# Kernel tuning notes

Hardware: AMD Instinct MI355X
Metric: run time of the kernel (lower is better)

The kernel has to match this reference:

```python
import jax, jax.numpy as jnp
import numpy as np

H, W = 448, 448
C = 32
HEADS = 2
HEAD_DIM = C // HEADS
B, N = 4, 20000
SHIFTS = jnp.array([[0, 0], [-1, 0], [1, 0], [0, 1], [-1, 1], [1, 1], [0, -1], [-1, -1], [1, -1]], dtype=jnp.int32)  # [9,2]


def _layer_norm(x, w, b):
    mu = x.mean(-1, keepdims=True)
    var = ((x - mu) ** 2).mean(-1, keepdims=True)
    return (x - mu) / jnp.sqrt(var + 1e-5) * w + b


def _direction(q_feat, q_coor, kv_feat, kv_coor, qkv_w, qkv_b, in_w, in_b, out_w, out_b, pos_w, pos_b):
    # q_feat: [N,C] (already layer-normed), q_coor/kv_coor: [N,2] int (y,x)
    n = q_feat.shape[0]
    q_map = q_feat @ qkv_w[0].T + qkv_b[0]   # 1x1 conv == linear
    k_map = kv_feat @ qkv_w[1].T + qkv_b[1]
    v_map = kv_feat @ qkv_w[2].T + qkv_b[2]
    # dense coordinate -> voxel-index lookup table for the kv modality
    lut = jnp.full(H * W, -1, dtype=jnp.int32)
    lut = lut.at[kv_coor[:, 0] * W + kv_coor[:, 1]].set(jnp.arange(kv_coor.shape[0], dtype=jnp.int32))
    shifted = q_coor[:, None, :] + SHIFTS[None]                      # [N,9,2]
    inb = ((shifted >= 0) & (shifted < jnp.array([H, W]))).all(-1)   # [N,9]
    flat = jnp.clip(shifted[..., 0], 0, H - 1) * W + jnp.clip(shifted[..., 1], 0, W - 1)
    idx = jnp.where(inb, lut[flat], -1)                              # [N,9], -1 = no match
    mask = idx >= 0
    gi = jnp.maximum(idx, 0)
    pos = SHIFTS.astype(q_feat.dtype) @ pos_w.T + pos_b              # [9,C]
    v_g = jnp.where(mask[..., None], v_map[gi] + pos[None], 0.0)     # [N,9,C]
    k_g = jnp.where(mask[..., None], k_map[gi], 0.0)                 # [N,9,C]
    # MultiheadAttention (eval): 1 query token over 9 neighbor tokens, per voxel
    wq, wk, wv = in_w[:C], in_w[C:2 * C], in_w[2 * C:]
    bq, bk, bv = in_b[:C], in_b[C:2 * C], in_b[2 * C:]
    q = (q_map @ wq.T + bq).reshape(n, HEADS, HEAD_DIM)
    k = (k_g @ wk.T + bk).reshape(n, 9, HEADS, HEAD_DIM)
    v = (v_g @ wv.T + bv).reshape(n, 9, HEADS, HEAD_DIM)
    scores = jnp.einsum('nhd,nkhd->nhk', q, k) / jnp.sqrt(jnp.asarray(HEAD_DIM, q.dtype))
    attn = jax.nn.softmax(scores, axis=-1)
    o = jnp.einsum('nhk,nkhd->nhd', attn, v).reshape(n, C)
    out = o @ out_w.T + out_b                                        # [N,C]
    # scatter into BEV pseudoimage
    canvas = jnp.zeros((H * W, C), out.dtype).at[q_coor[:, 0] * W + q_coor[:, 1]].set(out)
    return canvas.T.reshape(C, H, W)


def setup_inputs() -> dict:
    key = jax.random.key(0)
    ks = jax.random.split(key, 20)
    rng = np.random.default_rng(0)
    def coords(rng):
        flat = np.stack([rng.choice(H * W, size=N, replace=False) for _ in range(B)])
        return jnp.asarray(np.stack([flat // W, flat % W], axis=-1), dtype=jnp.int32)  # [B,N,2]
    s = 0.05
    return {
        'li_feats': jax.random.normal(ks[0], (B, N, C), jnp.float32),
        'ra_feats': jax.random.normal(ks[1], (B, N, C), jnp.float32),
        'li_coors': coords(rng),
        'ra_coors': coords(rng),
        'li_norm_w': jnp.ones((C,), jnp.float32),
        'li_norm_b': jnp.zeros((C,), jnp.float32),
        'ra_norm_w': jnp.ones((C,), jnp.float32),
        'ra_norm_b': jnp.zeros((C,), jnp.float32),
        'qkv1_w': jax.random.normal(ks[2], (3, C, C), jnp.float32) * s,
        'qkv1_b': jax.random.normal(ks[3], (3, C), jnp.float32) * s,
        'qkv2_w': jax.random.normal(ks[4], (3, C, C), jnp.float32) * s,
        'qkv2_b': jax.random.normal(ks[5], (3, C), jnp.float32) * s,
        'pos_w': jax.random.normal(ks[6], (C, 2), jnp.float32) * s,
        'pos_b': jax.random.normal(ks[7], (C,), jnp.float32) * s,
        'attn1_in_w': jax.random.normal(ks[8], (3 * C, C), jnp.float32) * s,
        'attn1_in_b': jax.random.normal(ks[9], (3 * C,), jnp.float32) * s,
        'attn1_out_w': jax.random.normal(ks[10], (C, C), jnp.float32) * s,
        'attn1_out_b': jax.random.normal(ks[11], (C,), jnp.float32) * s,
        'attn2_in_w': jax.random.normal(ks[12], (3 * C, C), jnp.float32) * s,
        'attn2_in_b': jax.random.normal(ks[13], (3 * C,), jnp.float32) * s,
        'attn2_out_w': jax.random.normal(ks[14], (C, C), jnp.float32) * s,
        'attn2_out_b': jax.random.normal(ks[15], (C,), jnp.float32) * s,
    }


def reference(li_feats, ra_feats, li_coors, ra_coors, li_norm_w, li_norm_b, ra_norm_w, ra_norm_b,
              qkv1_w, qkv1_b, qkv2_w, qkv2_b, pos_w, pos_b,
              attn1_in_w, attn1_in_b, attn1_out_w, attn1_out_b,
              attn2_in_w, attn2_in_b, attn2_out_w, attn2_out_b):
    li_n = _layer_norm(li_feats, li_norm_w, li_norm_b)  # [B,N,C]
    ra_n = _layer_norm(ra_feats, ra_norm_w, ra_norm_b)
    d1 = jax.vmap(lambda qf, qc, kf, kc: _direction(qf, qc, kf, kc, qkv1_w, qkv1_b,
                                                    attn1_in_w, attn1_in_b, attn1_out_w, attn1_out_b, pos_w, pos_b))
    d2 = jax.vmap(lambda qf, qc, kf, kc: _direction(qf, qc, kf, kc, qkv2_w, qkv2_b,
                                                    attn2_in_w, attn2_in_b, attn2_out_w, attn2_out_b, pos_w, pos_b))
    li_img = d1(li_n, li_coors, ra_n, ra_coors)  # [B,C,H,W]
    ra_img = d2(ra_n, ra_coors, li_n, li_coors)  # [B,C,H,W]
    return li_img, ra_img
```

## Files before the change

### kernel.cpp

```cpp
#include <hip/hip_runtime.h>
#include <hip/hip_bf16.h>

#define HH 448
#define WW 448
#define HWP (HH*WW)
#define CC 32
#define NN 20000
#define BB 4
#define PBLK 512
#define NPB 79

__constant__ int c_SY[9] = {0,-1,1,0,-1,1,0,-1,1};
__constant__ int c_SX[9] = {0,0,0,1,1,1,-1,-1,-1};

#define WB_STRIDE 4608

static __device__ __forceinline__ float bf(const __hip_bfloat16 v) {
    return __bfloat162float(v);
}
static __device__ __forceinline__ float ldf(const void* p, int i, int isf32) {
    if (isf32) return ((const float*)p)[i];
    return __bfloat162float(((const __hip_bfloat16*)p)[i]);
}
static __device__ __forceinline__ float blo(unsigned int u) { return __uint_as_float((u & 0xFFFFu) << 16); }
static __device__ __forceinline__ float bhi(unsigned int u) { return __uint_as_float(u & 0xFFFF0000u); }

static __device__ __forceinline__ void unpack8(uint4 r, float* f) {
    f[0]=blo(r.x); f[1]=bhi(r.x); f[2]=blo(r.y); f[3]=bhi(r.y);
    f[4]=blo(r.z); f[5]=bhi(r.z); f[6]=blo(r.w); f[7]=bhi(r.w);
}
static __device__ __forceinline__ float dot8(uint4 r, const float* q) {
    float a = 0.f;
    a = fmaf(blo(r.x), q[0], a); a = fmaf(bhi(r.x), q[1], a);
    a = fmaf(blo(r.y), q[2], a); a = fmaf(bhi(r.y), q[3], a);
    a = fmaf(blo(r.z), q[4], a); a = fmaf(bhi(r.z), q[5], a);
    a = fmaf(blo(r.w), q[6], a); a = fmaf(bhi(r.w), q[7], a);
    return a;
}
static __device__ __forceinline__ void acc8(uint4 r, float w, float4 pA, float4 pB, float* o) {
    o[0]=fmaf(w, blo(r.x)+pA.x, o[0]); o[1]=fmaf(w, bhi(r.x)+pA.y, o[1]);
    o[2]=fmaf(w, blo(r.y)+pA.z, o[2]); o[3]=fmaf(w, bhi(r.y)+pA.w, o[3]);
    o[4]=fmaf(w, blo(r.z)+pB.x, o[4]); o[5]=fmaf(w, bhi(r.z)+pB.y, o[5]);
    o[6]=fmaf(w, blo(r.w)+pB.z, o[6]); o[7]=fmaf(w, bhi(r.w)+pB.w, o[7]);
}

__launch_bounds__(256)
__global__ void prep_build(const void* __restrict__ qkv1_w, const void* __restrict__ qkv1_b,
                           const void* __restrict__ qkv2_w, const void* __restrict__ qkv2_b,
                           const void* __restrict__ pos_w,  const void* __restrict__ pos_b,
                           const void* __restrict__ in1_w,  const void* __restrict__ in1_b,
                           const void* __restrict__ out1_w, const void* __restrict__ out1_b,
                           const void* __restrict__ in2_w,  const void* __restrict__ in2_b,
                           const void* __restrict__ out2_w, const void* __restrict__ out2_b,
                           const void* __restrict__ li_feats,
                           const int* __restrict__ li_coors, const int* __restrict__ ra_coors,
                           int* __restrict__ lut,
                           int* __restrict__ flag, float* __restrict__ wsW) {
    const int tid = threadIdx.x;
    if (blockIdx.x >= 2) {
        const int t = (blockIdx.x - 2) * 256 + tid;
        if (t >= 2 * BB * NN) return;
        const int tensor = t / (BB * NN);
        const int r = t % (BB * NN);
        const int b = r / NN, n = r % NN;
        const int* cc = tensor ? ra_coors : li_coors;
        const int y = cc[(size_t)(b * NN + n) * 2 + 0];
        const int x = cc[(size_t)(b * NN + n) * 2 + 1];
        lut[(size_t)(tensor * BB + b) * HWP + y * WW + x] = n;
        return;
    }
    __shared__ int cnt[256];
    {
        const unsigned short u = ((const unsigned short*)li_feats)[tid * 2];
        const int e = (u >> 7) & 0xFF;
        cnt[tid] = (u == 0 || (e >= 97 && e <= 157)) ? 1 : 0;
    }
    __syncthreads();
    for (int s = 128; s > 0; s >>= 1) {
        if (tid < s) cnt[tid] += cnt[tid + s];
        __syncthreads();
    }
    const int F = (cnt[0] >= 192) ? 0 : 1;
    if (blockIdx.x == 0 && tid == 0) *flag = F;

    const int d = blockIdx.x;
    const void* qw  = d ? qkv2_w : qkv1_w;
    const void* qb  = d ? qkv2_b : qkv1_b;
    const void* iw  = d ? in2_w  : in1_w;
    const void* ib  = d ? in2_b  : in1_b;
    const void* ow  = d ? out2_w : out1_w;
    const void* obp = d ? out2_b : out1_b;
    float* o = wsW + d * WB_STRIDE;

    __shared__ float s_qw[3072];
    __shared__ float s_iw[96 * 33];
    __shared__ float s_ow[32 * 33];
    __shared__ float s_qb[96], s_ib[96], s_obp[32], s_pw[64], s_pb[32];

    if (F) {
        const float* fqw = (const float*)qw;  const float* fiw = (const float*)iw;
        const float* fow = (const float*)ow;  const float* fqb = (const float*)qb;
        const float* fib = (const float*)ib;  const float* fob = (const float*)obp;
        const float* fpw = (const float*)pos_w; const float* fpb = (const float*)pos_b;
        for (int i = tid; i < 3072; i += 256) s_qw[i] = fqw[i];
        for (int i = tid; i < 3072; i += 256) s_iw[(i >> 5) * 33 + (i & 31)] = fiw[i];
        for (int i = tid; i < 1024; i += 256) s_ow[(i >> 5) * 33 + (i & 31)] = fow[i];
        if (tid < 96) { s_qb[tid] = fqb[tid]; s_ib[tid] = fib[tid]; }
        if (tid < 64) s_pw[tid] = fpw[tid];
        if (tid < 32) { s_obp[tid] = fob[tid]; s_pb[tid] = fpb[tid]; }
    } else {
        const __hip_bfloat16* hqw = (const __hip_bfloat16*)qw;  const __hip_bfloat16* hiw = (const __hip_bfloat16*)iw;
        const __hip_bfloat16* how = (const __hip_bfloat16*)ow;  const __hip_bfloat16* hqb = (const __hip_bfloat16*)qb;
        const __hip_bfloat16* hib = (const __hip_bfloat16*)ib;  const __hip_bfloat16* hob = (const __hip_bfloat16*)obp;
        const __hip_bfloat16* hpw = (const __hip_bfloat16*)pos_w; const __hip_bfloat16* hpb = (const __hip_bfloat16*)pos_b;
        for (int i = tid; i < 3072; i += 256) s_qw[i] = bf(hqw[i]);
        for (int i = tid; i < 3072; i += 256) s_iw[(i >> 5) * 33 + (i & 31)] = bf(hiw[i]);
        for (int i = tid; i < 1024; i += 256) s_ow[(i >> 5) * 33 + (i & 31)] = bf(how[i]);
        if (tid < 96) { s_qb[tid] = bf(hqb[tid]); s_ib[tid] = bf(hib[tid]); }
        if (tid < 64) s_pw[tid] = bf(hpw[tid]);
        if (tid < 32) { s_obp[tid] = bf(hob[tid]); s_pb[tid] = bf(hpb[tid]); }
    }
    __syncthreads();

    for (int k = 0; k < 4; ++k) {
        const int idx = tid + k * 256;
        const int t = idx >> 5, i = idx & 31;
        float aq = 0.f, ak = 0.f, av = 0.f;
        #pragma unroll
        for (int u = 0; u < 32; ++u) {
            const float q0 = s_qw[u * 32 + t];
            const float q1 = s_qw[1024 + u * 32 + t];
            const float q2 = s_qw[2048 + u * 32 + t];
            aq = fmaf(s_iw[i * 33 + u],        q0, aq);
            ak = fmaf(s_iw[(32 + i) * 33 + u], q1, ak);
            av = fmaf(s_iw[(64 + i) * 33 + u], q2, av);
        }
        o[idx]        = aq;
        o[1024 + idx] = ak;
        o[2048 + idx] = av;
        o[3072 + idx] = s_ow[i * 33 + t];
    }
    if (tid < 32) {
        const int i = tid;
        float aq = 0.f, ak = 0.f, av = 0.f;
        #pragma unroll
        for (int u = 0; u < 32; ++u) {
            aq = fmaf(s_qb[u],      s_iw[i * 33 + u],        aq);
            ak = fmaf(s_qb[32 + u], s_iw[(32 + i) * 33 + u], ak);
            av = fmaf(s_qb[64 + u], s_iw[(64 + i) * 33 + u], av);
        }
        o[4096 + i] = aq + s_ib[i];
        o[4128 + i] = ak + s_ib[32 + i];
        o[4160 + i] = av + s_ib[64 + i];
        o[4192 + i] = s_obp[i];
        o[4224 + i] = s_ib[32 + i];
        o[4256 + i] = s_ib[64 + i];
    }
    for (int idx = tid; idx < 288; idx += 256) {
        const int s = idx >> 5, i = idx & 31;
        const float sy = (float)c_SY[s], sx = (float)c_SX[s];
        float acc = 0.f;
        #pragma unroll
        for (int j = 0; j < 32; ++j) {
            const float pj = sy * s_pw[j * 2 + 0] + sx * s_pw[j * 2 + 1] + s_pb[j];
            acc = fmaf(pj, s_iw[(64 + i) * 33 + j], acc);
        }
        o[4288 + idx] = acc;
    }
}

__launch_bounds__(256)
__global__ void project_kernel(const void* __restrict__ li_feats, const void* __restrict__ ra_feats,
                               const void* __restrict__ li_nw, const void* __restrict__ li_nb,
                               const void* __restrict__ ra_nw, const void* __restrict__ ra_nb,
                               const int* __restrict__ flag, const float* __restrict__ wsW,
                               __hip_bfloat16* __restrict__ qOut, __hip_bfloat16* __restrict__ kOut,
                               __hip_bfloat16* __restrict__ vOut) {
    const int F = *flag;
    const int combo  = blockIdx.x / PBLK;
    const int blk    = blockIdx.x % PBLK;
    const int tensor = combo >> 2;
    const int b      = combo & 3;
    const int qd  = tensor;
    const int kvd = 1 - tensor;

    __shared__ float wq[1024], wk[1024], wv[1024];
    __shared__ float bq[32], bk[32], bvv[32], nw[32], nb[32];
    const float* Wq  = wsW + qd  * WB_STRIDE;
    const float* Wkv = wsW + kvd * WB_STRIDE;
    for (int k = threadIdx.x; k < 1024; k += 256) {
        wq[k] = Wq[k];
        wk[k] = Wkv[1024 + k];
        wv[k] = Wkv[2048 + k];
    }
    if (threadIdx.x < 32) {
        bq[threadIdx.x]  = Wq[4096 + threadIdx.x];
        bk[threadIdx.x]  = Wkv[4128 + threadIdx.x];
        bvv[threadIdx.x] = Wkv[4160 + threadIdx.x];
        const void* w  = tensor ? ra_nw : li_nw;
        const void* bb = tensor ? ra_nb : li_nb;
        nw[threadIdx.x] = ldf(w, threadIdx.x, F);
        nb[threadIdx.x] = ldf(bb, threadIdx.x, F);
    }
    __syncthreads();

    const void* feats = tensor ? ra_feats : li_feats;
    const int lane = threadIdx.x & 31;
    const int sub  = threadIdx.x >> 5;

    for (int n0 = blk * 8; n0 < NN; n0 += PBLK * 8) {
        const int n = n0 + sub;
        if (n < NN) {
            const float x = ldf(feats, (b * NN + n) * CC + lane, F);
            float s = x;
            #pragma unroll
            for (int m = 1; m < 32; m <<= 1) s += __shfl_xor(s, m);
            const float mu = s * (1.f / 32.f);
            const float dx = x - mu;
            float s2 = dx * dx;
            #pragma unroll
            for (int m = 1; m < 32; m <<= 1) s2 += __shfl_xor(s2, m);
            const float var = s2 * (1.f / 32.f);
            const float xn = dx * rsqrtf(var + 1e-5f) * nw[lane] + nb[lane];

            float aq = bq[lane], ak = bk[lane], av = bvv[lane];
            #pragma unroll
            for (int t = 0; t < 32; ++t) {
                const float xb = __shfl(xn, t, 32);
                aq = fmaf(wq[t * 32 + lane], xb, aq);
                ak = fmaf(wk[t * 32 + lane], xb, ak);
                av = fmaf(wv[t * 32 + lane], xb, av);
            }
            const size_t off = ((size_t)(tensor * BB + b) * NN + n) * CC + lane;
            qOut[off] = __float2bfloat16(aq);
            kOut[off] = __float2bfloat16(ak);
            vOut[off] = __float2bfloat16(av);
        }
    }
}

__launch_bounds__(256)
__global__ void attn_kernel(const int* __restrict__ li_coors, const int* __restrict__ ra_coors,
                            const float* __restrict__ wsW, const int* __restrict__ lut,
                            const __hip_bfloat16* __restrict__ qArr, const __hip_bfloat16* __restrict__ kArr,
                            const __hip_bfloat16* __restrict__ vArr, __hip_bfloat16* __restrict__ resArr) {
    const int combo = blockIdx.x / NPB;
    const int n     = (blockIdx.x % NPB) * 256 + threadIdx.x;
    const int d = combo >> 2;
    const int b = combo & 3;
    const int qt = d, kt = 1 - d;

    __shared__ __align__(16) float wo[1024];
    __shared__ __align__(16) float pv[288];
    __shared__ __align__(16) float ob[32], bkr[32], bvr[32];
    const float* Wd = wsW + d * WB_STRIDE;
    for (int k = threadIdx.x; k < 1024; k += 256) wo[k] = Wd[3072 + k];
    if (threadIdx.x < 32) {
        ob[threadIdx.x]  = Wd[4192 + threadIdx.x];
        bkr[threadIdx.x] = Wd[4224 + threadIdx.x];
        bvr[threadIdx.x] = Wd[4256 + threadIdx.x];
    }
    for (int k = threadIdx.x; k < 288; k += 256) pv[k] = Wd[4288 + k];
    __syncthreads();
    if (n >= NN) return;

    const int* qc = qt ? ra_coors : li_coors;
    const int* lutk = lut + (size_t)(kt * BB + b) * HWP;
    const __hip_bfloat16* kk = kArr + (size_t)(kt * BB + b) * NN * CC;
    const __hip_bfloat16* vv = vArr + (size_t)(kt * BB + b) * NN * CC;
    const __hip_bfloat16* qq = qArr + (size_t)(qt * BB + b) * NN * CC;
    __hip_bfloat16* res = resArr + (size_t)(d * BB + b) * NN * CC;

    float q[32];
    {
        const uint4* qr = (const uint4*)(qq + (size_t)n * CC);
        unpack8(qr[0], q); unpack8(qr[1], q + 8);
        unpack8(qr[2], q + 16); unpack8(qr[3], q + 24);
    }
    const int y = qc[(size_t)(b * NN + n) * 2 + 0];
    const int x = qc[(size_t)(b * NN + n) * 2 + 1];
    int idx[9];
    #pragma unroll
    for (int s = 0; s < 9; ++s) {
        const int ny = y + c_SY[s], nx = x + c_SX[s];
        idx[s] = (ny >= 0 && ny < HH && nx >= 0 && nx < WW) ? lutk[ny * WW + nx] : -1;
    }
    float di0 = 0.f, di1 = 0.f;
    #pragma unroll
    for (int c = 0; c < 16; ++c) di0 = fmaf(q[c], bkr[c], di0);
    #pragma unroll
    for (int c = 16; c < 32; ++c) di1 = fmaf(q[c], bkr[c], di1);

    float s0[9], s1[9];
    #pragma unroll
    for (int s = 0; s < 9; ++s) {
        float d0, d1;
        if (idx[s] >= 0) {
            const uint4* kr = (const uint4*)(kk + (size_t)idx[s] * CC);
            const uint4 r0 = kr[0], r1 = kr[1], r2 = kr[2], r3 = kr[3];
            d0 = dot8(r0, q) + dot8(r1, q + 8);
            d1 = dot8(r2, q + 16) + dot8(r3, q + 24);
        } else { d0 = di0; d1 = di1; }
        s0[s] = d0 * 0.25f;
        s1[s] = d1 * 0.25f;
    }
    float m0 = s0[0], m1 = s1[0];
    #pragma unroll
    for (int s = 1; s < 9; ++s) { m0 = fmaxf(m0, s0[s]); m1 = fmaxf(m1, s1[s]); }
    float e0[9], e1[9], den0 = 0.f, den1 = 0.f;
    #pragma unroll
    for (int s = 0; s < 9; ++s) {
        e0[s] = __expf(s0[s] - m0); den0 += e0[s];
        e1[s] = __expf(s1[s] - m1); den1 += e1[s];
    }
    const float i0 = 1.f / den0, i1 = 1.f / den1;

    float o[32];
    #pragma unroll
    for (int c = 0; c < 32; ++c) o[c] = 0.f;
    float wi0 = 0.f, wi1 = 0.f;
    const float4* pv4 = (const float4*)pv;
    #pragma unroll
    for (int s = 0; s < 9; ++s) {
        const float w0 = e0[s] * i0, w1 = e1[s] * i1;
        if (idx[s] >= 0) {
            const uint4* vr = (const uint4*)(vv + (size_t)idx[s] * CC);
            const uint4 r0 = vr[0], r1 = vr[1], r2 = vr[2], r3 = vr[3];
            acc8(r0, w0, pv4[s * 8 + 0], pv4[s * 8 + 1], o);
            acc8(r1, w0, pv4[s * 8 + 2], pv4[s * 8 + 3], o + 8);
            acc8(r2, w1, pv4[s * 8 + 4], pv4[s * 8 + 5], o + 16);
            acc8(r3, w1, pv4[s * 8 + 6], pv4[s * 8 + 7], o + 24);
        } else { wi0 += w0; wi1 += w1; }
    }
    #pragma unroll
    for (int c = 0; c < 16; ++c) o[c] = fmaf(wi0, bvr[c], o[c]);
    #pragma unroll
    for (int c = 16; c < 32; ++c) o[c] = fmaf(wi1, bvr[c], o[c]);

    float out[32];
    const float4* ob4 = (const float4*)ob;
    #pragma unroll
    for (int i4 = 0; i4 < 8; ++i4) {
        const float4 t = ob4[i4];
        out[i4 * 4 + 0] = t.x; out[i4 * 4 + 1] = t.y;
        out[i4 * 4 + 2] = t.z; out[i4 * 4 + 3] = t.w;
    }
    #pragma unroll
    for (int j = 0; j < 32; ++j) {
        const float oj = o[j];
        const float4* wr = (const float4*)&wo[j * 32];
        #pragma unroll
        for (int i4 = 0; i4 < 8; ++i4) {
            const float4 w = wr[i4];
            out[i4 * 4 + 0] = fmaf(oj, w.x, out[i4 * 4 + 0]);
            out[i4 * 4 + 1] = fmaf(oj, w.y, out[i4 * 4 + 1]);
            out[i4 * 4 + 2] = fmaf(oj, w.z, out[i4 * 4 + 2]);
            out[i4 * 4 + 3] = fmaf(oj, w.w, out[i4 * 4 + 3]);
        }
    }
    __hip_bfloat16 hb[32];
    #pragma unroll
    for (int c = 0; c < 32; ++c) hb[c] = __float2bfloat16(out[c]);
    uint4* rp = (uint4*)(res + (size_t)n * CC);
    const uint4* hp = (const uint4*)hb;
    rp[0] = hp[0]; rp[1] = hp[1]; rp[2] = hp[2]; rp[3] = hp[3];
}

__launch_bounds__(256)
__global__ void canvas_kernel(const int* __restrict__ lut, const __hip_bfloat16* __restrict__ resArr,
                              const int* __restrict__ flag, void* __restrict__ out) {
    const int F = *flag;
    const int tile = blockIdx.x % (HWP / 64);
    const int rem  = blockIdx.x / (HWP / 64);
    const int b = rem & 3;
    const int d = rem >> 2;
    const int* lutq = lut + (size_t)(d * BB + b) * HWP + (size_t)tile * 64;
    __shared__ int ls[64];
    __shared__ float st[64 * 33];
    const int t = threadIdx.x;
    if (t < 16) ((int4*)ls)[t] = ((const int4*)lutq)[t];
    __syncthreads();

    const __hip_bfloat16* res = resArr + (size_t)(d * BB + b) * NN * CC;
    {
        const int r = t >> 2, q = t & 3;
        const int idx = ls[r];
        uint4 raw = make_uint4(0u, 0u, 0u, 0u);
        if (idx >= 0) raw = *(const uint4*)(res + (size_t)idx * CC + q * 8);
        float* dst = &st[r * 33 + q * 8];
        dst[0] = blo(raw.x); dst[1] = bhi(raw.x);
        dst[2] = blo(raw.y); dst[3] = bhi(raw.y);
        dst[4] = blo(raw.z); dst[5] = bhi(raw.z);
        dst[6] = blo(raw.w); dst[7] = bhi(raw.w);
    }
    __syncthreads();

    const int c = t >> 3, g = t & 7;
    float v[8];
    #pragma unroll
    for (int j = 0; j < 8; ++j) v[j] = st[(8 * g + j) * 33 + c];
    const size_t obase = ((size_t)(d * BB + b) * CC + c) * HWP + (size_t)tile * 64 + 8 * g;
    if (F) {
        float* ob = (float*)out + obase;
        ((float4*)ob)[0] = make_float4(v[0], v[1], v[2], v[3]);
        ((float4*)ob)[1] = make_float4(v[4], v[5], v[6], v[7]);
    } else {
        __hip_bfloat16* ob = (__hip_bfloat16*)out + obase;
        __hip_bfloat16 h[8];
        #pragma unroll
        for (int j = 0; j < 8; ++j) h[j] = __float2bfloat16(v[j]);
        *(uint4*)ob = *(const uint4*)h;
    }
}

extern "C" void kernel_launch(void* const* d_in, const int* in_sizes, int n_in,
                              void* d_out, int out_size, void* d_ws, size_t ws_size,
                              hipStream_t stream) {
    (void)in_sizes; (void)n_in; (void)out_size; (void)ws_size;
    const void* li_feats = d_in[0];
    const void* ra_feats = d_in[1];
    const int* li_coors = (const int*)d_in[2];
    const int* ra_coors = (const int*)d_in[3];
    const void* li_nw = d_in[4];
    const void* li_nb = d_in[5];
    const void* ra_nw = d_in[6];
    const void* ra_nb = d_in[7];

    char* ws = (char*)d_ws;
    int*   flag = (int*)ws;
    float* wsW  = (float*)(ws + 512);
    int*   lut  = (int*)(ws + 40960);
    __hip_bfloat16* qArr = (__hip_bfloat16*)(ws + 6463488);
    __hip_bfloat16* kArr = (__hip_bfloat16*)(ws + 16703488);
    __hip_bfloat16* vArr = (__hip_bfloat16*)(ws + 26943488);
    __hip_bfloat16* rArr = qArr;

    hipMemsetAsync(lut, 0xFF, (size_t)2 * BB * HWP * sizeof(int), stream);
    const int buildBlocks = (2 * BB * NN + 255) / 256;
    prep_build<<<2 + buildBlocks, 256, 0, stream>>>(d_in[8], d_in[9], d_in[10], d_in[11], d_in[12], d_in[13],
                                                    d_in[14], d_in[15], d_in[16], d_in[17],
                                                    d_in[18], d_in[19], d_in[20], d_in[21],
                                                    li_feats, li_coors, ra_coors, lut, flag, wsW);
    project_kernel<<<8 * PBLK, 256, 0, stream>>>(li_feats, ra_feats, li_nw, li_nb, ra_nw, ra_nb,
                                                 flag, wsW, qArr, kArr, vArr);
    attn_kernel<<<8 * NPB, 256, 0, stream>>>(li_coors, ra_coors, wsW, lut, qArr, kArr, vArr, rArr);
    canvas_kernel<<<2 * BB * (HWP / 64), 256, 0, stream>>>(lut, rArr, flag, d_out);
}
```

Baseline: 373.6 us.

## Map one voxel per thread in projection and read weights directly from global

```diff
diff --git a/kernel.cpp b/kernel.cpp
--- a/kernel.cpp
+++ b/kernel.cpp
@@ -7,7 +7,6 @@
 #define CC 32
 #define NN 20000
 #define BB 4
-#define PBLK 512
 #define NPB 79
 
 __constant__ int c_SY[9] = {0,-1,1,0,-1,1,0,-1,1};
@@ -42,6 +41,13 @@
     o[2]=fmaf(w, blo(r.y)+pA.z, o[2]); o[3]=fmaf(w, bhi(r.y)+pA.w, o[3]);
     o[4]=fmaf(w, blo(r.z)+pB.x, o[4]); o[5]=fmaf(w, bhi(r.z)+pB.y, o[5]);
     o[6]=fmaf(w, blo(r.w)+pB.z, o[6]); o[7]=fmaf(w, bhi(r.w)+pB.w, o[7]);
+}
+static __device__ __forceinline__ void store32bf(__hip_bfloat16* p, const float* a) {
+    __hip_bfloat16 h[32];
+    #pragma unroll
+    for (int c = 0; c < 32; ++c) h[c] = __float2bfloat16(a[c]);
+    uint4* rp = (uint4*)p; const uint4* hp = (const uint4*)h;
+    rp[0] = hp[0]; rp[1] = hp[1]; rp[2] = hp[2]; rp[3] = hp[3];
 }
 
 __launch_bounds__(256)
@@ -177,65 +183,69 @@
                                __hip_bfloat16* __restrict__ qOut, __hip_bfloat16* __restrict__ kOut,
                                __hip_bfloat16* __restrict__ vOut) {
     const int F = *flag;
-    const int combo  = blockIdx.x / PBLK;
-    const int blk    = blockIdx.x % PBLK;
+    const int combo  = blockIdx.x / NPB;
+    const int n      = (blockIdx.x % NPB) * 256 + threadIdx.x;
+    if (n >= NN) return;
     const int tensor = combo >> 2;
     const int b      = combo & 3;
-    const int qd  = tensor;
-    const int kvd = 1 - tensor;
-
-    __shared__ float wq[1024], wk[1024], wv[1024];
-    __shared__ float bq[32], bk[32], bvv[32], nw[32], nb[32];
-    const float* Wq  = wsW + qd  * WB_STRIDE;
-    const float* Wkv = wsW + kvd * WB_STRIDE;
-    for (int k = threadIdx.x; k < 1024; k += 256) {
-        wq[k] = Wq[k];
-        wk[k] = Wkv[1024 + k];
-        wv[k] = Wkv[2048 + k];
-    }
-    if (threadIdx.x < 32) {
-        bq[threadIdx.x]  = Wq[4096 + threadIdx.x];
-        bk[threadIdx.x]  = Wkv[4128 + threadIdx.x];
-        bvv[threadIdx.x] = Wkv[4160 + threadIdx.x];
-        const void* w  = tensor ? ra_nw : li_nw;
-        const void* bb = tensor ? ra_nb : li_nb;
-        nw[threadIdx.x] = ldf(w, threadIdx.x, F);
-        nb[threadIdx.x] = ldf(bb, threadIdx.x, F);
-    }
-    __syncthreads();
+    const float* Wq  = wsW + tensor * WB_STRIDE;
+    const float* Wkv = wsW + (1 - tensor) * WB_STRIDE;
 
     const void* feats = tensor ? ra_feats : li_feats;
-    const int lane = threadIdx.x & 31;
-    const int sub  = threadIdx.x >> 5;
-
-    for (int n0 = blk * 8; n0 < NN; n0 += PBLK * 8) {
-        const int n = n0 + sub;
-        if (n < NN) {
-            const float x = ldf(feats, (b * NN + n) * CC + lane, F);
-            float s = x;
+    const void* nwp   = tensor ? ra_nw : li_nw;
+    const void* nbp   = tensor ? ra_nb : li_nb;
+
+    float x[32];
+    if (F) {
+        const float4* fr = (const float4*)((const float*)feats + (size_t)(b * NN + n) * CC);
+        #pragma unroll
+        for (int i = 0; i < 8; ++i) {
+            const float4 t = fr[i];
+            x[4*i] = t.x; x[4*i+1] = t.y; x[4*i+2] = t.z; x[4*i+3] = t.w;
+        }
+    } else {
+        const uint4* hr = (const uint4*)((const __hip_bfloat16*)feats + (size_t)(b * NN + n) * CC);
+        unpack8(hr[0], x); unpack8(hr[1], x + 8);
+        unpack8(hr[2], x + 16); unpack8(hr[3], x + 24);
+    }
+    float s = 0.f;
+    #pragma unroll
+    for (int c = 0; c < 32; ++c) s += x[c];
+    const float mu = s * (1.f / 32.f);
+    float s2 = 0.f;
+    #pragma unroll
+    for (int c = 0; c < 32; ++c) { const float dx = x[c] - mu; s2 += dx * dx; }
+    const float rs = rsqrtf(s2 * (1.f / 32.f) + 1e-5f);
+    #pragma unroll
+    for (int c = 0; c < 32; ++c)
+        x[c] = (x[c] - mu) * rs * ldf(nwp, c, F) + ldf(nbp, c, F);
+
+    const size_t off = ((size_t)(tensor * BB + b) * NN + n) * CC;
+    #pragma unroll
+    for (int pass = 0; pass < 3; ++pass) {
+        const float* W = (pass == 0) ? Wq : Wkv + pass * 1024;
+        const float* Bv = (pass == 0) ? (Wq + 4096) : (Wkv + 4096 + pass * 32);
+        float a[32];
+        const float4* b4 = (const float4*)Bv;
+        #pragma unroll
+        for (int i4 = 0; i4 < 8; ++i4) {
+            const float4 t = b4[i4];
+            a[4*i4] = t.x; a[4*i4+1] = t.y; a[4*i4+2] = t.z; a[4*i4+3] = t.w;
+        }
+        #pragma unroll
+        for (int j = 0; j < 32; ++j) {
+            const float xj = x[j];
+            const float4* wr = (const float4*)&W[j * 32];
             #pragma unroll
-            for (int m = 1; m < 32; m <<= 1) s += __shfl_xor(s, m);
-            const float mu = s * (1.f / 32.f);
-            const float dx = x - mu;
-            float s2 = dx * dx;
-            #pragma unroll
-            for (int m = 1; m < 32; m <<= 1) s2 += __shfl_xor(s2, m);
-            const float var = s2 * (1.f / 32.f);
-            const float xn = dx * rsqrtf(var + 1e-5f) * nw[lane] + nb[lane];
-
-            float aq = bq[lane], ak = bk[lane], av = bvv[lane];
-            #pragma unroll
-            for (int t = 0; t < 32; ++t) {
-                const float xb = __shfl(xn, t, 32);
-                aq = fmaf(wq[t * 32 + lane], xb, aq);
-                ak = fmaf(wk[t * 32 + lane], xb, ak);
-                av = fmaf(wv[t * 32 + lane], xb, av);
+            for (int i4 = 0; i4 < 8; ++i4) {
+                const float4 w = wr[i4];
+                a[4*i4+0] = fmaf(xj, w.x, a[4*i4+0]);
+                a[4*i4+1] = fmaf(xj, w.y, a[4*i4+1]);
+                a[4*i4+2] = fmaf(xj, w.z, a[4*i4+2]);
+                a[4*i4+3] = fmaf(xj, w.w, a[4*i4+3]);
             }
-            const size_t off = ((size_t)(tensor * BB + b) * NN + n) * CC + lane;
-            qOut[off] = __float2bfloat16(aq);
-            kOut[off] = __float2bfloat16(ak);
-            vOut[off] = __float2bfloat16(av);
-        }
+        }
+        store32bf((pass == 0 ? qOut : pass == 1 ? kOut : vOut) + off, a);
     }
 }
 
@@ -246,23 +256,11 @@
                             const __hip_bfloat16* __restrict__ vArr, __hip_bfloat16* __restrict__ resArr) {
     const int combo = blockIdx.x / NPB;
     const int n     = (blockIdx.x % NPB) * 256 + threadIdx.x;
+    if (n >= NN) return;
     const int d = combo >> 2;
     const int b = combo & 3;
     const int qt = d, kt = 1 - d;
-
-    __shared__ __align__(16) float wo[1024];
-    __shared__ __align__(16) float pv[288];
-    __shared__ __align__(16) float ob[32], bkr[32], bvr[32];
     const float* Wd = wsW + d * WB_STRIDE;
-    for (int k = threadIdx.x; k < 1024; k += 256) wo[k] = Wd[3072 + k];
-    if (threadIdx.x < 32) {
-        ob[threadIdx.x]  = Wd[4192 + threadIdx.x];
-        bkr[threadIdx.x] = Wd[4224 + threadIdx.x];
-        bvr[threadIdx.x] = Wd[4256 + threadIdx.x];
-    }
-    for (int k = threadIdx.x; k < 288; k += 256) pv[k] = Wd[4288 + k];
-    __syncthreads();
-    if (n >= NN) return;
 
     const int* qc = qt ? ra_coors : li_coors;
     const int* lutk = lut + (size_t)(kt * BB + b) * HWP;
@@ -287,9 +285,9 @@
     }
     float di0 = 0.f, di1 = 0.f;
     #pragma unroll
-    for (int c = 0; c < 16; ++c) di0 = fmaf(q[c], bkr[c], di0);
-    #pragma unroll
-    for (int c = 16; c < 32; ++c) di1 = fmaf(q[c], bkr[c], di1);
+    for (int c = 0; c < 16; ++c) di0 = fmaf(q[c], Wd[4224 + c], di0);
+    #pragma unroll
+    for (int c = 16; c < 32; ++c) di1 = fmaf(q[c], Wd[4224 + c], di1);
 
     float s0[9], s1[9];
     #pragma unroll
@@ -319,7 +317,7 @@
     #pragma unroll
     for (int c = 0; c < 32; ++c) o[c] = 0.f;
     float wi0 = 0.f, wi1 = 0.f;
-    const float4* pv4 = (const float4*)pv;
+    const float4* pv4 = (const float4*)&Wd[4288];
     #pragma unroll
     for (int s = 0; s < 9; ++s) {
         const float w0 = e0[s] * i0, w1 = e1[s] * i1;
@@ -333,37 +331,32 @@
         } else { wi0 += w0; wi1 += w1; }
     }
     #pragma unroll
-    for (int c = 0; c < 16; ++c) o[c] = fmaf(wi0, bvr[c], o[c]);
-    #pragma unroll
-    for (int c = 16; c < 32; ++c) o[c] = fmaf(wi1, bvr[c], o[c]);
+    for (int c = 0; c < 16; ++c) o[c] = fmaf(wi0, Wd[4256 + c], o[c]);
+    #pragma unroll
+    for (int c = 16; c < 32; ++c) o[c] = fmaf(wi1, Wd[4256 + c], o[c]);
 
     float out[32];
-    const float4* ob4 = (const float4*)ob;
+    const float4* ob4 = (const float4*)&Wd[4192];
     #pragma unroll
     for (int i4 = 0; i4 < 8; ++i4) {
         const float4 t = ob4[i4];
-        out[i4 * 4 + 0] = t.x; out[i4 * 4 + 1] = t.y;
-        out[i4 * 4 + 2] = t.z; out[i4 * 4 + 3] = t.w;
+        out[i4*4+0] = t.x; out[i4*4+1] = t.y;
+        out[i4*4+2] = t.z; out[i4*4+3] = t.w;
     }
     #pragma unroll
     for (int j = 0; j < 32; ++j) {
         const float oj = o[j];
-        const float4* wr = (const float4*)&wo[j * 32];
+        const float4* wr = (const float4*)&Wd[3072 + j * 32];
         #pragma unroll
         for (int i4 = 0; i4 < 8; ++i4) {
             const float4 w = wr[i4];
-            out[i4 * 4 + 0] = fmaf(oj, w.x, out[i4 * 4 + 0]);
-            out[i4 * 4 + 1] = fmaf(oj, w.y, out[i4 * 4 + 1]);
-            out[i4 * 4 + 2] = fmaf(oj, w.z, out[i4 * 4 + 2]);
-            out[i4 * 4 + 3] = fmaf(oj, w.w, out[i4 * 4 + 3]);
-        }
-    }
-    __hip_bfloat16 hb[32];
-    #pragma unroll
-    for (int c = 0; c < 32; ++c) hb[c] = __float2bfloat16(out[c]);
-    uint4* rp = (uint4*)(res + (size_t)n * CC);
-    const uint4* hp = (const uint4*)hb;
-    rp[0] = hp[0]; rp[1] = hp[1]; rp[2] = hp[2]; rp[3] = hp[3];
+            out[i4*4+0] = fmaf(oj, w.x, out[i4*4+0]);
+            out[i4*4+1] = fmaf(oj, w.y, out[i4*4+1]);
+            out[i4*4+2] = fmaf(oj, w.z, out[i4*4+2]);
+            out[i4*4+3] = fmaf(oj, w.w, out[i4*4+3]);
+        }
+    }
+    store32bf(res + (size_t)n * CC, out);
 }
 
 __launch_bounds__(256)
@@ -433,7 +426,7 @@
     __hip_bfloat16* qArr = (__hip_bfloat16*)(ws + 6463488);
     __hip_bfloat16* kArr = (__hip_bfloat16*)(ws + 16703488);
     __hip_bfloat16* vArr = (__hip_bfloat16*)(ws + 26943488);
-    __hip_bfloat16* rArr = qArr;
+    __hip_bfloat16* rArr = (__hip_bfloat16*)(ws + 37183488);
 
     hipMemsetAsync(lut, 0xFF, (size_t)2 * BB * HWP * sizeof(int), stream);
     const int buildBlocks = (2 * BB * NN + 255) / 256;
@@ -441,8 +434,8 @@
                                                     d_in[14], d_in[15], d_in[16], d_in[17],
                                                     d_in[18], d_in[19], d_in[20], d_in[21],
                                                     li_feats, li_coors, ra_coors, lut, flag, wsW);
-    project_kernel<<<8 * PBLK, 256, 0, stream>>>(li_feats, ra_feats, li_nw, li_nb, ra_nw, ra_nb,
-                                                 flag, wsW, qArr, kArr, vArr);
+    project_kernel<<<8 * NPB, 256, 0, stream>>>(li_feats, ra_feats, li_nw, li_nb, ra_nw, ra_nb,
+                                                flag, wsW, qArr, kArr, vArr);
     attn_kernel<<<8 * NPB, 256, 0, stream>>>(li_coors, ra_coors, wsW, lut, qArr, kArr, vArr, rArr);
     canvas_kernel<<<2 * BB * (HWP / 64), 256, 0, stream>>>(lut, rArr, flag, d_out);
 }
```

New measurement: 334.9 us, median of 2. -10.4%, faster.
